# Optimization experiments

Measured on AMD Instinct MI355X. Metric: run time of the kernel, lower is better.

The kernel has to match this reference:

```python
import jax, jax.numpy as jnp
import numpy as np

B, LQ, LK = 4, 2048, 2048
DIM = 1024          # intermediate_dim
H, D = 16, 64       # num_heads, head_dim
AD = H * D          # attn_dim
SCALE = 1.0 / np.sqrt(D).astype(np.float32)


def setup_inputs() -> dict:
    key = jax.random.key(0)
    ks = jax.random.split(key, 12)
    init = lambda k, shape, fan_in: jax.random.normal(k, shape, jnp.float32) / np.sqrt(fan_in).astype(np.float32)
    return {
        "x": jax.random.normal(ks[0], (B, LQ, DIM), jnp.float32),
        "embeds": jax.random.normal(ks[1], (B, LK, DIM), jnp.float32),
        "Wq": init(ks[2], (DIM, AD), DIM), "bq": jnp.zeros((AD,), jnp.float32),
        "Wk": init(ks[3], (DIM, AD), DIM), "bk": jnp.zeros((AD,), jnp.float32),
        "Wv": init(ks[4], (DIM, AD), DIM), "bv": jnp.zeros((AD,), jnp.float32),
        "Wo": init(ks[5], (AD, DIM), AD), "bo": jnp.zeros((DIM,), jnp.float32),
    }


def reference(x, embeds, Wq, bq, Wk, bk, Wv, bv, Wo, bo):
    b, lq, _ = x.shape
    lk = embeds.shape[1]
    # separate QKV projections (cross-attention: K,V from embeds)
    q = (x @ Wq + bq).reshape(b, lq, H, D)
    k = (embeds @ Wk + bk).reshape(b, lk, H, D)
    v = (embeds @ Wv + bv).reshape(b, lk, H, D)
    # scaled dot-product attention; full [b,h,lq,lk] score matrix (as in source)
    scores = jnp.einsum("bqhd,bkhd->bhqk", q, k) * SCALE
    attn = jax.nn.softmax(scores, axis=-1)  # dropout is identity at eval
    ctx = jnp.einsum("bhqk,bkhd->bqhd", attn, v).reshape(b, lq, AD)
    return ctx @ Wo + bo
```

## Files before the change

### kernel.cpp

```cpp
#include <hip/hip_runtime.h>
#include <cstdint>
#include <cstddef>

#define NB   4
#define NLQ  2048
#define NLK  2048
#define NDIM 1024
#define NH   16
#define ND   64
#define NAD  1024

typedef __attribute__((ext_vector_type(8))) short bf16x8;
typedef __attribute__((ext_vector_type(4))) short sh4;
typedef __attribute__((ext_vector_type(4))) float f32x4;
typedef __attribute__((ext_vector_type(4))) int   i32x4;

static __device__ __forceinline__ short f2bf(float f) {
    unsigned u = __builtin_bit_cast(unsigned, f);
    u += 0x7fffu + ((u >> 16) & 1u);
    return (short)(u >> 16);
}

#define GLL16(GP, LP) __builtin_amdgcn_global_load_lds( \
    (const __attribute__((address_space(1))) void*)(GP), \
    (__attribute__((address_space(3))) void*)(LP), 16, 0, 0)

__global__ void cvt2(const float* __restrict__ x, const float* __restrict__ e,
                     short* __restrict__ xo, short* __restrict__ eo) {
    const float* in = blockIdx.y ? e : x;
    short* out = blockIdx.y ? eo : xo;
    int i = (blockIdx.x * blockDim.x + threadIdx.x) * 4;
    const float4 v = *(const float4*)(in + i);
    sh4 o;
    o.x = f2bf(v.x); o.y = f2bf(v.y); o.z = f2bf(v.z); o.w = f2bf(v.w);
    *(sh4*)(out + i) = o;
}

__global__ void wtrans4(const float* __restrict__ W0, const float* __restrict__ W1,
                        const float* __restrict__ W2, const float* __restrict__ W3,
                        short* __restrict__ T0, short* __restrict__ T1,
                        short* __restrict__ T2, short* __restrict__ T3) {
    __shared__ float t[32][33];
    const int z = blockIdx.z;
    const float* W = (z == 0) ? W0 : (z == 1) ? W1 : (z == 2) ? W2 : W3;
    short* Wt = (z == 0) ? T0 : (z == 1) ? T1 : (z == 2) ? T2 : T3;
    const int bx = blockIdx.x * 32;
    const int by = blockIdx.y * 32;
    const int tx = threadIdx.x & 31, ty = threadIdx.x >> 5;
    #pragma unroll
    for (int i = 0; i < 32; i += 8)
        t[ty + i][tx] = W[(size_t)(bx + ty + i) * 1024 + by + tx];
    __syncthreads();
    #pragma unroll
    for (int i = 0; i < 32; i += 8)
        Wt[(size_t)(by + ty + i) * 1024 + bx + tx] = f2bf(t[tx][ty + i]);
}

__global__ void vtrans(const short* __restrict__ V, short* __restrict__ Vt) {
    __shared__ __align__(16) short T[64 * 72];
    const int s0 = blockIdx.x * 64;
    const int h = blockIdx.y, b = blockIdx.z;
    const int tid = threadIdx.x;
    const int sr = tid >> 3, c = tid & 7;
    #pragma unroll
    for (int i = 0; i < 2; ++i) {
        const int s = i * 32 + sr;
        const bf16x8 v = *(const bf16x8*)(V + (size_t)(b * NLK + s0 + s) * NAD + h * 64 + c * 8);
        #pragma unroll
        for (int j = 0; j < 8; ++j)
            T[(c * 8 + j) * 72 + s] = v[j];
    }
    __syncthreads();
    #pragma unroll
    for (int i = 0; i < 2; ++i) {
        const int d = i * 32 + sr;
        const bf16x8 o = *(const bf16x8*)&T[d * 72 + c * 8];
        *(bf16x8*)(Vt + ((size_t)((b * NH + h) * 64 + d)) * NLK + s0 + c * 8) = o;
    }
}

__global__ __launch_bounds__(256) void gemm_qkv(const short* __restrict__ Xb,
                                                const short* __restrict__ Eb,
                                                const short* __restrict__ Wqt,
                                                const short* __restrict__ Wkt,
                                                const short* __restrict__ Wvt,
                                                const float* __restrict__ bq,
                                                const float* __restrict__ bk,
                                                const float* __restrict__ bv,
                                                short* __restrict__ Qb,
                                                short* __restrict__ Kf,
                                                short* __restrict__ Vb)
{
    const int N = 1024, K = 1024;
    __shared__ __align__(16) short As[128 * 32];
    __shared__ __align__(16) short Bs[128 * 32];
    const int z = blockIdx.z;
    const short* A    = (z == 0) ? Xb : Eb;
    const short* Wt   = (z == 0) ? Wqt : (z == 1) ? Wkt : Wvt;
    const float* bias = (z == 0) ? bq : (z == 1) ? bk : bv;
    const float scale = (z == 0) ? 0.18033688011112042f : 1.0f;

    const int tid = threadIdx.x, wave = tid >> 6, lane = tid & 63;
    const int quad = lane >> 4, col = lane & 15;
    const int m0 = blockIdx.x * 128, n0 = blockIdx.y * 128;
    const int wm = wave >> 1, wn = wave & 1;

    const f32x4 zero = {0.f, 0.f, 0.f, 0.f};
    f32x4 acc[4][4];
    #pragma unroll
    for (int i = 0; i < 4; ++i)
        #pragma unroll
        for (int j = 0; j < 4; ++j)
            acc[i][j] = zero;

    for (int kt = 0; kt < K / 32; ++kt) {
        __syncthreads();
        #pragma unroll
        for (int i = 0; i < 2; ++i) {
            const int f = (i * 4 + wave) * 512 + lane * 8;
            const int r = f >> 5, c = f & 31;
            GLL16(A  + (size_t)(m0 + r) * K + kt * 32 + c, &As[f]);
            GLL16(Wt + (size_t)(n0 + r) * K + kt * 32 + c, &Bs[f]);
        }
        __syncthreads();
        bf16x8 af[4], bfr[4];
        #pragma unroll
        for (int mt = 0; mt < 4; ++mt)
            af[mt] = *(const bf16x8*)&As[(wm * 64 + mt * 16 + col) * 32 + quad * 8];
        #pragma unroll
        for (int nt = 0; nt < 4; ++nt)
            bfr[nt] = *(const bf16x8*)&Bs[(wn * 64 + nt * 16 + col) * 32 + quad * 8];
        #pragma unroll
        for (int mt = 0; mt < 4; ++mt)
            #pragma unroll
            for (int nt = 0; nt < 4; ++nt)
                acc[mt][nt] = __builtin_amdgcn_mfma_f32_16x16x32_bf16(af[mt], bfr[nt], acc[mt][nt], 0, 0, 0);
    }

    short* outp = (z == 0) ? Qb : (z == 1) ? Kf : Vb;
    #pragma unroll
    for (int mt = 0; mt < 4; ++mt)
        #pragma unroll
        for (int nt = 0; nt < 4; ++nt) {
            const int n = n0 + wn * 64 + nt * 16 + col;
            const float bv_ = bias[n];
            #pragma unroll
            for (int r = 0; r < 4; ++r) {
                const int m = m0 + wm * 64 + mt * 16 + quad * 4 + r;
                outp[(size_t)m * N + n] = f2bf((acc[mt][nt][r] + bv_) * scale);
            }
        }
}

__global__ __launch_bounds__(256) void gemm_out(const short* __restrict__ A,
                                                const short* __restrict__ Wt,
                                                const float* __restrict__ bias,
                                                float* __restrict__ outp)
{
    const int N = 1024, K = 1024;
    __shared__ __align__(16) short As[128 * 32];
    __shared__ __align__(16) short Bs[128 * 32];
    const int tid = threadIdx.x, wave = tid >> 6, lane = tid & 63;
    const int quad = lane >> 4, col = lane & 15;
    const int m0 = blockIdx.x * 128, n0 = blockIdx.y * 128;
    const int wm = wave >> 1, wn = wave & 1;

    const f32x4 zero = {0.f, 0.f, 0.f, 0.f};
    f32x4 acc[4][4];
    #pragma unroll
    for (int i = 0; i < 4; ++i)
        #pragma unroll
        for (int j = 0; j < 4; ++j)
            acc[i][j] = zero;

    for (int kt = 0; kt < K / 32; ++kt) {
        __syncthreads();
        #pragma unroll
        for (int i = 0; i < 2; ++i) {
            const int f = (i * 4 + wave) * 512 + lane * 8;
            const int r = f >> 5, c = f & 31;
            GLL16(A  + (size_t)(m0 + r) * K + kt * 32 + c, &As[f]);
            GLL16(Wt + (size_t)(n0 + r) * K + kt * 32 + c, &Bs[f]);
        }
        __syncthreads();
        bf16x8 af[4], bfr[4];
        #pragma unroll
        for (int mt = 0; mt < 4; ++mt)
            af[mt] = *(const bf16x8*)&As[(wm * 64 + mt * 16 + col) * 32 + quad * 8];
        #pragma unroll
        for (int nt = 0; nt < 4; ++nt)
            bfr[nt] = *(const bf16x8*)&Bs[(wn * 64 + nt * 16 + col) * 32 + quad * 8];
        #pragma unroll
        for (int mt = 0; mt < 4; ++mt)
            #pragma unroll
            for (int nt = 0; nt < 4; ++nt)
                acc[mt][nt] = __builtin_amdgcn_mfma_f32_16x16x32_bf16(af[mt], bfr[nt], acc[mt][nt], 0, 0, 0);
    }

    #pragma unroll
    for (int mt = 0; mt < 4; ++mt)
        #pragma unroll
        for (int nt = 0; nt < 4; ++nt) {
            const int n = n0 + wn * 64 + nt * 16 + col;
            const float bv_ = bias[n];
            #pragma unroll
            for (int r = 0; r < 4; ++r) {
                const int m = m0 + wm * 64 + mt * 16 + quad * 4 + r;
                outp[(size_t)m * N + n] = acc[mt][nt][r] + bv_;
            }
        }
}

__global__ __launch_bounds__(256, 2) void attn_fused5(const short* __restrict__ Q,
                                                      const short* __restrict__ Kb,
                                                      const short* __restrict__ Vt,
                                                      short* __restrict__ ctx)
{
    __shared__ __align__(16) short Ks[64 * 64];
    __shared__ __align__(16) short Vs[64 * 64];
    const int tid = threadIdx.x, wave = tid >> 6, lane = tid & 63;
    const int quad = lane >> 4, col = lane & 15;
    const int h = blockIdx.y, b = blockIdx.z;
    const int q0 = blockIdx.x * 256 + wave * 64;

    bf16x8 aq[4][2];
    #pragma unroll
    for (int mt = 0; mt < 4; ++mt) {
        const short* qp = Q + (size_t)(b * NLQ + q0 + mt * 16 + col) * NAD + h * 64 + quad * 8;
        aq[mt][0] = *(const bf16x8*)qp;
        aq[mt][1] = *(const bf16x8*)(qp + 32);
    }

    const f32x4 zero = {0.f, 0.f, 0.f, 0.f};
    f32x4 O[4][4];
    float lp[4];
    #pragma unroll
    for (int mt = 0; mt < 4; ++mt) {
        lp[mt] = 0.f;
        #pragma unroll
        for (int db = 0; db < 4; ++db) O[db][mt] = zero;
    }

    const int srow = tid >> 3, schunk = tid & 7;
    const short* kbase = Kb + (size_t)b * NLK * NAD + h * 64 + schunk * 8;
    const short* vbase = Vt + (size_t)(b * NH + h) * 64 * NLK + schunk * 8;

    bf16x8 kv[2], vv[2];
    #pragma unroll
    for (int i = 0; i < 2; ++i) {
        const int row = i * 32 + srow;
        kv[i] = *(const bf16x8*)(kbase + (size_t)row * NAD);
        vv[i] = *(const bf16x8*)(vbase + (size_t)row * NLK);
    }

    for (int kt = 0; kt < NLK / 64; ++kt) {
        __syncthreads();
        #pragma unroll
        for (int i = 0; i < 2; ++i) {
            const int row = i * 32 + srow;
            const int c = (schunk ^ (row & 7)) * 8;
            *(bf16x8*)&Ks[row * 64 + c] = kv[i];
            *(bf16x8*)&Vs[row * 64 + c] = vv[i];
        }
        __syncthreads();

        const int nk = (kt + 1) & (NLK / 64 - 1);
        #pragma unroll
        for (int i = 0; i < 2; ++i) {
            const int row = i * 32 + srow;
            kv[i] = *(const bf16x8*)(kbase + (size_t)(nk * 64 + row) * NAD);
            vv[i] = *(const bf16x8*)(vbase + (size_t)row * NLK + nk * 64);
        }

        bf16x8 kf[2][4];
        #pragma unroll
        for (int kk = 0; kk < 2; ++kk)
            #pragma unroll
            for (int nt = 0; nt < 4; ++nt) {
                const int key = nt * 16 + col;
                kf[kk][nt] = *(const bf16x8*)&Ks[key * 64 + (((kk * 4 + quad) ^ (key & 7)) * 8)];
            }

        int pk[4][2][4];
        #pragma unroll
        for (int mt = 0; mt < 4; ++mt) {
            f32x4 st[4];
            #pragma unroll
            for (int nt = 0; nt < 4; ++nt) st[nt] = zero;
            #pragma unroll
            for (int kk = 0; kk < 2; ++kk)
                #pragma unroll
                for (int nt = 0; nt < 4; ++nt)
                    st[nt] = __builtin_amdgcn_mfma_f32_16x16x32_bf16(kf[kk][nt], aq[mt][kk], st[nt], 0, 0, 0);
            #pragma unroll
            for (int nt = 0; nt < 4; ++nt) {
                unsigned u[4];
                #pragma unroll
                for (int r = 0; r < 4; ++r) {
                    u[r] = __builtin_bit_cast(unsigned, __builtin_amdgcn_exp2f(st[nt][r]));
                    lp[mt] += __builtin_bit_cast(float, u[r] & 0xffff0000u);
                }
                const int t = nt >> 1, odd = (nt & 1) * 2;
                pk[mt][t][odd + 0] = (u[0] >> 16) | (u[1] & 0xffff0000u);
                pk[mt][t][odd + 1] = (u[2] >> 16) | (u[3] & 0xffff0000u);
            }
        }

        #pragma unroll
        for (int t = 0; t < 2; ++t)
            #pragma unroll
            for (int db = 0; db < 4; ++db) {
                const int row = db * 16 + col;
                const int c0 = t * 32 + quad * 4;
                const int c1 = t * 32 + 16 + quad * 4;
                const sh4 lo = *(const sh4*)&Vs[row * 64 + (((c0 >> 3) ^ (row & 7)) * 8 + (c0 & 7))];
                const sh4 hi = *(const sh4*)&Vs[row * 64 + (((c1 >> 3) ^ (row & 7)) * 8 + (c1 & 7))];
                bf16x8 va;
                #pragma unroll
                for (int j = 0; j < 4; ++j) { va[j] = lo[j]; va[j + 4] = hi[j]; }
                #pragma unroll
                for (int mt = 0; mt < 4; ++mt) {
                    const bf16x8 pb = __builtin_bit_cast(bf16x8,
                        i32x4{pk[mt][t][0], pk[mt][t][1], pk[mt][t][2], pk[mt][t][3]});
                    O[db][mt] = __builtin_amdgcn_mfma_f32_16x16x32_bf16(va, pb, O[db][mt], 0, 0, 0);
                }
            }
    }

    #pragma unroll
    for (int mt = 0; mt < 4; ++mt) {
        float l = lp[mt];
        l += __shfl_xor(l, 16, 64);
        l += __shfl_xor(l, 32, 64);
        const float linv = 1.0f / l;
        #pragma unroll
        for (int db = 0; db < 4; ++db) {
            sh4 o4;
            #pragma unroll
            for (int r = 0; r < 4; ++r)
                o4[r] = f2bf(O[db][mt][r] * linv);
            short* cp = ctx + (size_t)(b * NLQ + q0 + mt * 16 + col) * NAD
                      + h * 64 + db * 16 + quad * 4;
            *(sh4*)cp = o4;
        }
    }
}

extern "C" void kernel_launch(void* const* d_in, const int* in_sizes, int n_in,
                              void* d_out, int out_size, void* d_ws, size_t ws_size,
                              hipStream_t stream)
{
    (void)in_sizes; (void)n_in; (void)out_size; (void)ws_size;
    const float* x  = (const float*)d_in[0];
    const float* e  = (const float*)d_in[1];
    const float* Wq = (const float*)d_in[2];
    const float* bq = (const float*)d_in[3];
    const float* Wk = (const float*)d_in[4];
    const float* bk = (const float*)d_in[5];
    const float* Wv = (const float*)d_in[6];
    const float* bv = (const float*)d_in[7];
    const float* Wo = (const float*)d_in[8];
    const float* bo = (const float*)d_in[9];
    float* out = (float*)d_out;

    const size_t MQ = (size_t)NB * NLQ;
    short* wsp = (short*)d_ws;
    short* Xb  = wsp;
    short* Eb  = Xb  + MQ * NDIM;
    short* Wqt = Eb  + MQ * NDIM;
    short* Wkt = Wqt + (size_t)NDIM * NAD;
    short* Wvt = Wkt + (size_t)NDIM * NAD;
    short* Wot = Wvt + (size_t)NDIM * NAD;
    short* Qb  = Wot + (size_t)NDIM * NAD;
    short* Kf  = Qb  + MQ * NAD;
    short* Vb  = Kf  + MQ * NAD;
    short* Vtb = Vb  + MQ * NAD;
    short* Cx  = Vtb + MQ * NAD;

    cvt2<<<dim3(8192, 2), 256, 0, stream>>>(x, e, Xb, Eb);
    wtrans4<<<dim3(32, 32, 4), 256, 0, stream>>>(Wq, Wk, Wv, Wo, Wqt, Wkt, Wvt, Wot);

    gemm_qkv<<<dim3(64, 8, 3), 256, 0, stream>>>(Xb, Eb, Wqt, Wkt, Wvt,
                                                 bq, bk, bv, Qb, Kf, Vb);

    vtrans<<<dim3(NLK / 64, NH, NB), 256, 0, stream>>>(Vb, Vtb);

    attn_fused5<<<dim3(NLQ / 256, NH, NB), 256, 0, stream>>>(Qb, Kf, Vtb, Cx);

    gemm_out<<<dim3(64, 8), 256, 0, stream>>>(Cx, Wot, bo, out);
}
```

Baseline: 303.6 us.

## Fuse V transpose into QKV GEMM epilogue, widen GEMM K-tile, MFMA row sums

The QKV GEMM now writes V directly in transposed per-head layout, which removes the separate vtrans kernel and its extra read/write of V. Both GEMMs use a 64-wide K tile with XOR-swizzled shared-memory layout, which halves the number of barriers and should reduce LDS bank conflicts. In attention, the softmax row sum is computed with an MFMA against a ones vector rather than scalar adds plus cross-lane shuffles, and bf16 packing uses a byte-permute instruction. The trade-offs are strided 8-byte scattered stores in the V epilogue and double the shared memory per GEMM block.

```diff
diff --git a/kernel.cpp b/kernel.cpp
--- a/kernel.cpp
+++ b/kernel.cpp
@@ -56,28 +56,6 @@
         Wt[(size_t)(by + ty + i) * 1024 + bx + tx] = f2bf(t[tx][ty + i]);
 }
 
-__global__ void vtrans(const short* __restrict__ V, short* __restrict__ Vt) {
-    __shared__ __align__(16) short T[64 * 72];
-    const int s0 = blockIdx.x * 64;
-    const int h = blockIdx.y, b = blockIdx.z;
-    const int tid = threadIdx.x;
-    const int sr = tid >> 3, c = tid & 7;
-    #pragma unroll
-    for (int i = 0; i < 2; ++i) {
-        const int s = i * 32 + sr;
-        const bf16x8 v = *(const bf16x8*)(V + (size_t)(b * NLK + s0 + s) * NAD + h * 64 + c * 8);
-        #pragma unroll
-        for (int j = 0; j < 8; ++j)
-            T[(c * 8 + j) * 72 + s] = v[j];
-    }
-    __syncthreads();
-    #pragma unroll
-    for (int i = 0; i < 2; ++i) {
-        const int d = i * 32 + sr;
-        const bf16x8 o = *(const bf16x8*)&T[d * 72 + c * 8];
-        *(bf16x8*)(Vt + ((size_t)((b * NH + h) * 64 + d)) * NLK + s0 + c * 8) = o;
-    }
-}
 
 __global__ __launch_bounds__(256) void gemm_qkv(const short* __restrict__ Xb,
                                                 const short* __restrict__ Eb,
@@ -89,11 +67,11 @@
                                                 const float* __restrict__ bv,
                                                 short* __restrict__ Qb,
                                                 short* __restrict__ Kf,
-                                                short* __restrict__ Vb)
+                                                short* __restrict__ Vtb)
 {
     const int N = 1024, K = 1024;
-    __shared__ __align__(16) short As[128 * 32];
-    __shared__ __align__(16) short Bs[128 * 32];
+    __shared__ __align__(16) short As[128 * 64];
+    __shared__ __align__(16) short Bs[128 * 64];
     const int z = blockIdx.z;
     const short* A    = (z == 0) ? Xb : Eb;
     const short* Wt   = (z == 0) ? Wqt : (z == 1) ? Wkt : Wvt;
@@ -113,43 +91,69 @@
         for (int j = 0; j < 4; ++j)
             acc[i][j] = zero;
 
-    for (int kt = 0; kt < K / 32; ++kt) {
-        __syncthreads();
-        #pragma unroll
-        for (int i = 0; i < 2; ++i) {
+    for (int kt = 0; kt < K / 64; ++kt) {
+        __syncthreads();
+        #pragma unroll
+        for (int i = 0; i < 4; ++i) {
             const int f = (i * 4 + wave) * 512 + lane * 8;
-            const int r = f >> 5, c = f & 31;
-            GLL16(A  + (size_t)(m0 + r) * K + kt * 32 + c, &As[f]);
-            GLL16(Wt + (size_t)(n0 + r) * K + kt * 32 + c, &Bs[f]);
-        }
-        __syncthreads();
-        bf16x8 af[4], bfr[4];
+            const int row = f >> 6, ch = (f >> 3) & 7;
+            const int gcol = kt * 64 + ((ch ^ (row & 7)) * 8);
+            GLL16(A  + (size_t)(m0 + row) * K + gcol, &As[f]);
+            GLL16(Wt + (size_t)(n0 + row) * K + gcol, &Bs[f]);
+        }
+        __syncthreads();
+        #pragma unroll
+        for (int kk = 0; kk < 2; ++kk) {
+            bf16x8 af[4], bfr[4];
+            #pragma unroll
+            for (int mt = 0; mt < 4; ++mt) {
+                const int r = wm * 64 + mt * 16 + col;
+                af[mt] = *(const bf16x8*)&As[r * 64 + (((kk * 4 + quad) ^ (r & 7)) * 8)];
+            }
+            #pragma unroll
+            for (int nt = 0; nt < 4; ++nt) {
+                const int r = wn * 64 + nt * 16 + col;
+                bfr[nt] = *(const bf16x8*)&Bs[r * 64 + (((kk * 4 + quad) ^ (r & 7)) * 8)];
+            }
+            #pragma unroll
+            for (int mt = 0; mt < 4; ++mt)
+                #pragma unroll
+                for (int nt = 0; nt < 4; ++nt)
+                    acc[mt][nt] = __builtin_amdgcn_mfma_f32_16x16x32_bf16(af[mt], bfr[nt], acc[mt][nt], 0, 0, 0);
+        }
+    }
+
+    if (z < 2) {
+        short* outp = (z == 0) ? Qb : Kf;
         #pragma unroll
         for (int mt = 0; mt < 4; ++mt)
-            af[mt] = *(const bf16x8*)&As[(wm * 64 + mt * 16 + col) * 32 + quad * 8];
-        #pragma unroll
-        for (int nt = 0; nt < 4; ++nt)
-            bfr[nt] = *(const bf16x8*)&Bs[(wn * 64 + nt * 16 + col) * 32 + quad * 8];
+            #pragma unroll
+            for (int nt = 0; nt < 4; ++nt) {
+                const int n = n0 + wn * 64 + nt * 16 + col;
+                const float bv_ = bias[n];
+                #pragma unroll
+                for (int r = 0; r < 4; ++r) {
+                    const int m = m0 + wm * 64 + mt * 16 + quad * 4 + r;
+                    outp[(size_t)m * N + n] = f2bf((acc[mt][nt][r] + bv_) * scale);
+                }
+            }
+    } else {
         #pragma unroll
         for (int mt = 0; mt < 4; ++mt)
             #pragma unroll
-            for (int nt = 0; nt < 4; ++nt)
-                acc[mt][nt] = __builtin_amdgcn_mfma_f32_16x16x32_bf16(af[mt], bfr[nt], acc[mt][nt], 0, 0, 0);
-    }
-
-    short* outp = (z == 0) ? Qb : (z == 1) ? Kf : Vb;
-    #pragma unroll
-    for (int mt = 0; mt < 4; ++mt)
-        #pragma unroll
-        for (int nt = 0; nt < 4; ++nt) {
-            const int n = n0 + wn * 64 + nt * 16 + col;
-            const float bv_ = bias[n];
-            #pragma unroll
-            for (int r = 0; r < 4; ++r) {
-                const int m = m0 + wm * 64 + mt * 16 + quad * 4 + r;
-                outp[(size_t)m * N + n] = f2bf((acc[mt][nt][r] + bv_) * scale);
-            }
-        }
+            for (int nt = 0; nt < 4; ++nt) {
+                const int n = n0 + wn * 64 + nt * 16 + col;
+                const int hh = n >> 6, d = n & 63;
+                const float bv_ = bias[n];
+                const int mb = m0 + wm * 64 + mt * 16 + quad * 4;
+                const int bb = mb >> 11, s = mb & 2047;
+                sh4 o4;
+                #pragma unroll
+                for (int r = 0; r < 4; ++r)
+                    o4[r] = f2bf(acc[mt][nt][r] + bv_);
+                *(sh4*)&Vtb[((size_t)((bb * NH + hh) * 64 + d)) * NLK + s] = o4;
+            }
+    }
 }
 
 __global__ __launch_bounds__(256) void gemm_out(const short* __restrict__ A,
@@ -158,8 +162,8 @@
                                                 float* __restrict__ outp)
 {
     const int N = 1024, K = 1024;
-    __shared__ __align__(16) short As[128 * 32];
-    __shared__ __align__(16) short Bs[128 * 32];
+    __shared__ __align__(16) short As[128 * 64];
+    __shared__ __align__(16) short Bs[128 * 64];
     const int tid = threadIdx.x, wave = tid >> 6, lane = tid & 63;
     const int quad = lane >> 4, col = lane & 15;
     const int m0 = blockIdx.x * 128, n0 = blockIdx.y * 128;
@@ -173,28 +177,36 @@
         for (int j = 0; j < 4; ++j)
             acc[i][j] = zero;
 
-    for (int kt = 0; kt < K / 32; ++kt) {
-        __syncthreads();
-        #pragma unroll
-        for (int i = 0; i < 2; ++i) {
+    for (int kt = 0; kt < K / 64; ++kt) {
+        __syncthreads();
+        #pragma unroll
+        for (int i = 0; i < 4; ++i) {
             const int f = (i * 4 + wave) * 512 + lane * 8;
-            const int r = f >> 5, c = f & 31;
-            GLL16(A  + (size_t)(m0 + r) * K + kt * 32 + c, &As[f]);
-            GLL16(Wt + (size_t)(n0 + r) * K + kt * 32 + c, &Bs[f]);
-        }
-        __syncthreads();
-        bf16x8 af[4], bfr[4];
-        #pragma unroll
-        for (int mt = 0; mt < 4; ++mt)
-            af[mt] = *(const bf16x8*)&As[(wm * 64 + mt * 16 + col) * 32 + quad * 8];
-        #pragma unroll
-        for (int nt = 0; nt < 4; ++nt)
-            bfr[nt] = *(const bf16x8*)&Bs[(wn * 64 + nt * 16 + col) * 32 + quad * 8];
-        #pragma unroll
-        for (int mt = 0; mt < 4; ++mt)
-            #pragma unroll
-            for (int nt = 0; nt < 4; ++nt)
-                acc[mt][nt] = __builtin_amdgcn_mfma_f32_16x16x32_bf16(af[mt], bfr[nt], acc[mt][nt], 0, 0, 0);
+            const int row = f >> 6, ch = (f >> 3) & 7;
+            const int gcol = kt * 64 + ((ch ^ (row & 7)) * 8);
+            GLL16(A  + (size_t)(m0 + row) * K + gcol, &As[f]);
+            GLL16(Wt + (size_t)(n0 + row) * K + gcol, &Bs[f]);
+        }
+        __syncthreads();
+        #pragma unroll
+        for (int kk = 0; kk < 2; ++kk) {
+            bf16x8 af[4], bfr[4];
+            #pragma unroll
+            for (int mt = 0; mt < 4; ++mt) {
+                const int r = wm * 64 + mt * 16 + col;
+                af[mt] = *(const bf16x8*)&As[r * 64 + (((kk * 4 + quad) ^ (r & 7)) * 8)];
+            }
+            #pragma unroll
+            for (int nt = 0; nt < 4; ++nt) {
+                const int r = wn * 64 + nt * 16 + col;
+                bfr[nt] = *(const bf16x8*)&Bs[r * 64 + (((kk * 4 + quad) ^ (r & 7)) * 8)];
+            }
+            #pragma unroll
+            for (int mt = 0; mt < 4; ++mt)
+                #pragma unroll
+                for (int nt = 0; nt < 4; ++nt)
+                    acc[mt][nt] = __builtin_amdgcn_mfma_f32_16x16x32_bf16(af[mt], bfr[nt], acc[mt][nt], 0, 0, 0);
+        }
     }
 
     #pragma unroll
@@ -211,7 +223,7 @@
         }
 }
 
-__global__ __launch_bounds__(256, 2) void attn_fused5(const short* __restrict__ Q,
+__global__ __launch_bounds__(256, 2) void attn_fused6(const short* __restrict__ Q,
                                                       const short* __restrict__ Kb,
                                                       const short* __restrict__ Vt,
                                                       short* __restrict__ ctx)
@@ -231,12 +243,16 @@
         aq[mt][1] = *(const bf16x8*)(qp + 32);
     }
 
+    bf16x8 vones;
+    #pragma unroll
+    for (int j = 0; j < 8; ++j) vones[j] = (short)0x3F80;
+
     const f32x4 zero = {0.f, 0.f, 0.f, 0.f};
     f32x4 O[4][4];
-    float lp[4];
+    f32x4 Ol[4];
     #pragma unroll
     for (int mt = 0; mt < 4; ++mt) {
-        lp[mt] = 0.f;
+        Ol[mt] = zero;
         #pragma unroll
         for (int db = 0; db < 4; ++db) O[db][mt] = zero;
     }
@@ -294,15 +310,19 @@
                     st[nt] = __builtin_amdgcn_mfma_f32_16x16x32_bf16(kf[kk][nt], aq[mt][kk], st[nt], 0, 0, 0);
             #pragma unroll
             for (int nt = 0; nt < 4; ++nt) {
-                unsigned u[4];
-                #pragma unroll
-                for (int r = 0; r < 4; ++r) {
-                    u[r] = __builtin_bit_cast(unsigned, __builtin_amdgcn_exp2f(st[nt][r]));
-                    lp[mt] += __builtin_bit_cast(float, u[r] & 0xffff0000u);
-                }
+                const unsigned u0 = __builtin_bit_cast(unsigned, __builtin_amdgcn_exp2f(st[nt][0]));
+                const unsigned u1 = __builtin_bit_cast(unsigned, __builtin_amdgcn_exp2f(st[nt][1]));
+                const unsigned u2 = __builtin_bit_cast(unsigned, __builtin_amdgcn_exp2f(st[nt][2]));
+                const unsigned u3 = __builtin_bit_cast(unsigned, __builtin_amdgcn_exp2f(st[nt][3]));
                 const int t = nt >> 1, odd = (nt & 1) * 2;
-                pk[mt][t][odd + 0] = (u[0] >> 16) | (u[1] & 0xffff0000u);
-                pk[mt][t][odd + 1] = (u[2] >> 16) | (u[3] & 0xffff0000u);
+                pk[mt][t][odd + 0] = (int)__builtin_amdgcn_perm(u1, u0, 0x07060302u);
+                pk[mt][t][odd + 1] = (int)__builtin_amdgcn_perm(u3, u2, 0x07060302u);
+            }
+            #pragma unroll
+            for (int t = 0; t < 2; ++t) {
+                const bf16x8 pb = __builtin_bit_cast(bf16x8,
+                    i32x4{pk[mt][t][0], pk[mt][t][1], pk[mt][t][2], pk[mt][t][3]});
+                Ol[mt] = __builtin_amdgcn_mfma_f32_16x16x32_bf16(vones, pb, Ol[mt], 0, 0, 0);
             }
         }
 
@@ -329,10 +349,7 @@
 
     #pragma unroll
     for (int mt = 0; mt < 4; ++mt) {
-        float l = lp[mt];
-        l += __shfl_xor(l, 16, 64);
-        l += __shfl_xor(l, 32, 64);
-        const float linv = 1.0f / l;
+        const float linv = 1.0f / Ol[mt][0];
         #pragma unroll
         for (int db = 0; db < 4; ++db) {
             sh4 o4;
@@ -373,19 +390,16 @@
     short* Wot = Wvt + (size_t)NDIM * NAD;
     short* Qb  = Wot + (size_t)NDIM * NAD;
     short* Kf  = Qb  + MQ * NAD;
-    short* Vb  = Kf  + MQ * NAD;
-    short* Vtb = Vb  + MQ * NAD;
+    short* Vtb = Kf  + MQ * NAD;
     short* Cx  = Vtb + MQ * NAD;
 
     cvt2<<<dim3(8192, 2), 256, 0, stream>>>(x, e, Xb, Eb);
     wtrans4<<<dim3(32, 32, 4), 256, 0, stream>>>(Wq, Wk, Wv, Wo, Wqt, Wkt, Wvt, Wot);
 
     gemm_qkv<<<dim3(64, 8, 3), 256, 0, stream>>>(Xb, Eb, Wqt, Wkt, Wvt,
-                                                 bq, bk, bv, Qb, Kf, Vb);
-
-    vtrans<<<dim3(NLK / 64, NH, NB), 256, 0, stream>>>(Vb, Vtb);
-
-    attn_fused5<<<dim3(NLQ / 256, NH, NB), 256, 0, stream>>>(Qb, Kf, Vtb, Cx);
+                                                 bq, bk, bv, Qb, Kf, Vtb);
+
+    attn_fused6<<<dim3(NLQ / 256, NH, NB), 256, 0, stream>>>(Qb, Kf, Vtb, Cx);
 
     gemm_out<<<dim3(64, 8), 256, 0, stream>>>(Cx, Wot, bo, out);
 }
```

Result: faster. 295.4 us (-2.7%).
